# Performance work log

Measured on AMD Instinct MI355X. Metric: run time of the kernel, lower is better.

Reference implementation:

```python
import jax, jax.numpy as jnp
import numpy as np

N, E, IN_DIM, HID, HEADS, OUT_DIM, T = 50000, 200000, 32, 64, 4, 32, 3
NEG_SLOPE = 0.2  # PyG GATv2Conv default


def setup_inputs() -> dict:
    key = jax.random.key(0)
    ks = jax.random.split(key, 16)
    s = 0.1
    return {
        "feat": jax.random.normal(ks[0], (N, IN_DIM), jnp.float32),
        "W_in": jax.random.normal(ks[1], (IN_DIM, HID), jnp.float32) * s,
        "b_in": jnp.zeros((HID,), jnp.float32),
        "Wl": jax.random.normal(ks[2], (2 * HID, HEADS * HID), jnp.float32) * s,
        "bl": jnp.zeros((HEADS * HID,), jnp.float32),
        "Wr": jax.random.normal(ks[3], (2 * HID, HEADS * HID), jnp.float32) * s,
        "br": jnp.zeros((HEADS * HID,), jnp.float32),
        "att": jax.random.normal(ks[4], (HEADS, HID), jnp.float32) * s,
        "b_conv": jnp.zeros((HEADS * HID,), jnp.float32),
        "Wg": jax.random.normal(ks[5], (HID, OUT_DIM), jnp.float32) * s,
        "bg": jnp.zeros((OUT_DIM,), jnp.float32),
        "edge_index": jax.random.randint(ks[6], (2, E), 0, N, jnp.int32),
        "node_mask": jax.random.randint(ks[7], (N,), 0, T + 1, jnp.int32),
        "current_state": jax.random.randint(ks[8], (N,), 0, 2, jnp.int32),
    }


def reference(feat, W_in, b_in, Wl, bl, Wr, br, att, b_conv, Wg, bg,
              edge_index, node_mask, current_state):
    # add self loops (GATv2Conv add_self_loops=True)
    loops = jnp.arange(N, dtype=edge_index.dtype)
    src = jnp.concatenate([edge_index[0], loops])  # [E+N]
    dst = jnp.concatenate([edge_index[1], loops])

    h0 = feat @ W_in + b_in  # [N, HID]
    bias_sum = b_conv.reshape(HEADS, HID).sum(0)  # heads are summed after bias add

    def step(h, i):
        active = node_mask > i  # [N] bool: nodes updated at this step
        x = jnp.concatenate([h, h0], axis=-1)  # [N, 2*HID]
        xl = (x @ Wl + bl).reshape(N, HEADS, HID)  # source transform
        xr = (x @ Wr + br).reshape(N, HEADS, HID)  # target transform
        e_act = active[src] & active[dst]  # edge alive iff both endpoints active
        s = jax.nn.leaky_relu(xl[src] + xr[dst], NEG_SLOPE)  # [E+N, H, C]
        score = jnp.einsum('ehc,hc->eh', s, att)  # [E+N, H]
        score = jnp.where(e_act[:, None], score, -1e30)
        smax = jax.lax.stop_gradient(
            jax.ops.segment_max(score, dst, num_segments=N))  # [N, H]
        ex = jnp.exp(score - smax[dst]) * e_act[:, None].astype(score.dtype)
        denom = jax.ops.segment_sum(ex, dst, num_segments=N)  # [N, H]
        alpha = ex / jnp.maximum(denom[dst], 1e-16)  # segment softmax per dst
        msg = alpha[:, :, None] * xl[src]  # [E+N, H, C]
        agg = jax.ops.segment_sum(msg, dst, num_segments=N)  # [N, H, C]
        out = jnp.tanh(agg.sum(1) + bias_sum)  # sum over heads, then Tanh
        return jnp.where(active[:, None], out, h), None

    h, _ = jax.lax.scan(step, h0, jnp.arange(T))
    # original returns g_embed(h[current_state]); fixed-shape variant: mask rows
    out = (h @ Wg + bg) * (current_state[:, None] > 0).astype(h.dtype)
    return out
```

## Files before the change

### kernel.cpp

```cpp
#include <hip/hip_runtime.h>
#include <hip/hip_bf16.h>

#define NN      50000
#define EE      200000
#define IN_DIM  32
#define HID     64
#define HEADS   4
#define OUTD    32
#define TSTEPS  3

typedef unsigned short bf16_t;
typedef __attribute__((ext_vector_type(8))) short  short8;
typedef __attribute__((ext_vector_type(4))) float  floatx4;

__device__ __forceinline__ float b2f(bf16_t u) {
    union { unsigned int i; float f; } v; v.i = ((unsigned int)u) << 16; return v.f;
}
__device__ __forceinline__ bf16_t f2b(float f) {
    union { float f; unsigned int i; } v; v.f = f;
    unsigned int r = v.i + 0x7FFF + ((v.i >> 16) & 1);
    return (bf16_t)(r >> 16);
}

#define H0_BLOCKS ((NN + 31) / 32)

__global__ __launch_bounds__(256) void k_setup(
        const void* W_in, const void* b_in, const void* att, const void* bconv,
        const void* Wg, const void* bg,
        const void* Wl_raw, const void* Wr_raw, const void* bl_raw, const void* br_raw,
        const void* feat_raw,
        float* attf, float* bcf, float* Wgf, float* bgf,
        bf16_t* __restrict__ Wt, bf16_t* __restrict__ WtS, float* __restrict__ bb,
        int* __restrict__ deg, int* __restrict__ flag, int* __restrict__ mbuf,
        bf16_t* __restrict__ h0, bf16_t* __restrict__ h) {
    __shared__ int bad;
    __shared__ float Ws[IN_DIM * HID];
    __shared__ float bs[HID];
    int t = threadIdx.x, bid = blockIdx.x;
    if (t == 0) bad = 0;
    __syncthreads();
    {
        const bf16_t* p = (const bf16_t*)W_in;
        int mybad = 0;
        for (int i = t; i < IN_DIM * HID; i += 256) {
            float v = b2f(p[i]);
            if (v != v || fabsf(v) > 100.f) mybad = 1;
        }
        if (mybad) atomicOr(&bad, 1);
    }
    __syncthreads();
    int f = bad ? 0 : 1;
    if (bid == 0 && t == 0) *flag = f;

    if (bid < 256) {
        int i = bid * 256 + t;
        int n = i >> 7, k = i & 127;
        const void* W = (n < 256) ? Wl_raw : Wr_raw;
        int nn = (n < 256) ? n : n - 256;
        float v = f ? b2f(((const bf16_t*)W)[k * 256 + nn])
                    : ((const float*)W)[k * 256 + nn];
        Wt[n * 128 + k] = f2b(v);
        if (k < 64) {
            float v2 = f ? b2f(((const bf16_t*)W)[(k + 64) * 256 + nn])
                         : ((const float*)W)[(k + 64) * 256 + nn];
            WtS[n * 64 + k] = f2b(v + v2);
        }
        if (k == 0) {
            const void* b = (n < 256) ? bl_raw : br_raw;
            bb[n] = f ? b2f(((const bf16_t*)b)[nn]) : ((const float*)b)[nn];
        }
    } else if (bid < 267) {
        int i = (bid - 256) * 256 + t;
        const void* src; float* dst; int off;
        if      (i < 256)  { src = att;   dst = attf; off = i; }
        else if (i < 512)  { src = bconv; dst = bcf;  off = i - 256; }
        else if (i < 2560) { src = Wg;    dst = Wgf;  off = i - 512; }
        else if (i < 2592) { src = bg;    dst = bgf;  off = i - 2560; }
        else return;
        dst[off] = f ? b2f(((const bf16_t*)src)[off]) : ((const float*)src)[off];
    } else if (bid < 463) {
        int i = (bid - 267) * 256 + t;
        if (i < NN) deg[i] = 0;
        if (bid == 267 && t < 16) mbuf[t] = 0;
    } else {
        for (int i = t; i < IN_DIM * HID; i += 256)
            Ws[i] = f ? b2f(((const bf16_t*)W_in)[i]) : ((const float*)W_in)[i];
        if (t < HID)
            bs[t] = f ? b2f(((const bf16_t*)b_in)[t]) : ((const float*)b_in)[t];
        __syncthreads();
        int nb = bid - 463;
        int wid = t >> 6, c = t & 63;
#pragma unroll
        for (int g = 0; g < 8; g++) {
            int node = (nb * 8 + g) * 4 + wid;
            if (node >= NN) break;
            float acc = bs[c];
            if (f) {
                const bf16_t* fr = (const bf16_t*)feat_raw + (size_t)node * IN_DIM;
#pragma unroll
                for (int k = 0; k < IN_DIM; k++) acc += b2f(fr[k]) * Ws[k * HID + c];
            } else {
                const float* fr = (const float*)feat_raw + (size_t)node * IN_DIM;
#pragma unroll
                for (int k = 0; k < IN_DIM; k++) acc += fr[k] * Ws[k * HID + c];
            }
            bf16_t o = f2b(acc);
            h0[(size_t)node * HID + c] = o;
            h [(size_t)node * HID + c] = o;
        }
    }
}

__global__ __launch_bounds__(256) void k_hist_all(const int* __restrict__ dst,
                                                  const int* __restrict__ mask,
                                                  int* __restrict__ deg,
                                                  int* __restrict__ mbuf) {
    int t = threadIdx.x, bid = blockIdx.x;
    int i = bid * 256 + t;
    if (i < EE) atomicAdd(&deg[dst[i]], 1);
    if (bid < (NN + 255) / 256) {
        __shared__ int wcnt[4][4];
        int wid = t >> 6, lane = t & 63;
        int ni = bid * 256 + t;
        bool valid = ni < NN;
        int v = 0;
        if (valid) { int m = mask[ni]; v = m < 0 ? 0 : (m > 3 ? 3 : m); }
#pragma unroll
        for (int b = 0; b < 4; b++) {
            unsigned long long mm = __ballot(valid && v == b);
            if (lane == 0) wcnt[wid][b] = __popcll(mm);
        }
        __syncthreads();
        if (t < 4) {
            int s = wcnt[0][t] + wcnt[1][t] + wcnt[2][t] + wcnt[3][t];
            if (s) atomicAdd(&mbuf[t], s);
        }
    }
}

__global__ __launch_bounds__(256) void k_scan_partial(const int* __restrict__ deg,
                                                      int* __restrict__ part, int n) {
    __shared__ int sd[256];
    int t = threadIdx.x;
    int base = blockIdx.x * 1024;
    int s = 0;
#pragma unroll
    for (int j = 0; j < 4; j++) {
        int i = base + t * 4 + j;
        if (i < n) s += deg[i];
    }
    sd[t] = s; __syncthreads();
    for (int off = 128; off > 0; off >>= 1) {
        if (t < off) sd[t] += sd[t + off];
        __syncthreads();
    }
    if (t == 0) part[blockIdx.x] = sd[0];
}

__global__ __launch_bounds__(256) void k_scan_final(const int* __restrict__ deg,
                                                    const int* __restrict__ part,
                                                    int* __restrict__ row_ptr,
                                                    int* __restrict__ cursor,
                                                    int n, int nch,
                                                    int* __restrict__ mbuf) {
    __shared__ int sc[256];
    __shared__ int bpref;
    int t = threadIdx.x;
    int bid = blockIdx.x;
    if (t == 0) {
        int acc = 0;
        for (int i = 0; i < bid; i++) acc += part[i];
        bpref = acc;
        if (bid == 0) {
            int tot = 0;
            for (int i = 0; i < nch; i++) tot += part[i];
            row_ptr[n] = tot;
            int c1 = mbuf[1], c2 = mbuf[2], c3 = mbuf[3];
            mbuf[7] = 0;
            mbuf[6] = c3;
            mbuf[5] = c3 + c2;
            mbuf[4] = c3 + c2 + c1;
            mbuf[8] = c3 + c2 + c1;
            mbuf[9] = c3 + c2;
            mbuf[10] = c3;
        }
    }
    int base = bid * 1024;
    int v[4]; int s = 0;
#pragma unroll
    for (int j = 0; j < 4; j++) {
        int i = base + t * 4 + j;
        v[j] = (i < n) ? deg[i] : 0;
        s += v[j];
    }
    sc[t] = s; __syncthreads();
    for (int off = 1; off < 256; off <<= 1) {
        int add = (t >= off) ? sc[t - off] : 0;
        __syncthreads();
        sc[t] += add;
        __syncthreads();
    }
    int run = sc[t] - s + bpref;
#pragma unroll
    for (int j = 0; j < 4; j++) {
        int i = base + t * 4 + j;
        if (i < n) { row_ptr[i] = run; cursor[i] = run; run += v[j]; }
    }
}

__global__ __launch_bounds__(256) void k_scatter_all(const int* __restrict__ src,
                                                     const int* __restrict__ dst,
                                                     int* __restrict__ cursor,
                                                     int* __restrict__ col,
                                                     const int* __restrict__ mask,
                                                     int* __restrict__ mbuf,
                                                     int* __restrict__ order) {
    int t = threadIdx.x, bid = blockIdx.x;
    int i = bid * 256 + t;
    if (i < EE) {
        int sv = src[i];
        int m = mask[sv]; m = m < 0 ? 0 : (m > 3 ? 3 : m);
        int d = dst[i];
        int pos = atomicAdd(&cursor[d], 1);
        col[pos] = sv | (m << 28);
    }
    if (bid < (NN + 255) / 256) {
        __shared__ int wcnt[4][4];
        __shared__ int bbase[4];
        int wid = t >> 6, lane = t & 63;
        int ni = bid * 256 + t;
        bool valid = ni < NN;
        int v = 0;
        if (valid) { int m = mask[ni]; v = m < 0 ? 0 : (m > 3 ? 3 : m); }
        int rank = 0;
#pragma unroll
        for (int b = 0; b < 4; b++) {
            unsigned long long mm = __ballot(valid && v == b);
            if (valid && v == b)
                rank = __popcll(mm & ((lane == 0) ? 0ull : (~0ull >> (64 - lane))));
            if (lane == 0) wcnt[wid][b] = __popcll(mm);
        }
        __syncthreads();
        if (t < 4) {
            int tot = wcnt[0][t] + wcnt[1][t] + wcnt[2][t] + wcnt[3][t];
            bbase[t] = atomicAdd(&mbuf[4 + t], tot);
        }
        __syncthreads();
        if (valid) {
            int wpre = 0;
            for (int ww = 0; ww < wid; ww++) wpre += wcnt[ww][v];
            order[bbase[v] + wpre + rank] = ni;
        }
    }
}

__global__ __launch_bounds__(256) void k_gemm0(const bf16_t* __restrict__ h0,
                                               const bf16_t* __restrict__ WtS,
                                               const float* __restrict__ bb,
                                               bf16_t* __restrict__ xl,
                                               bf16_t* __restrict__ xr,
                                               const int* __restrict__ order,
                                               const int* __restrict__ mbuf) {
    int count = mbuf[8];
    int mbase = blockIdx.x * 64;
    if (mbase >= count) return;

    __shared__ bf16_t smem[64 * 72 + 128 * 72];
    bf16_t* As = smem;
    bf16_t* Bs = smem + 64 * 72;
    bf16_t* Cs = smem;

    int t = threadIdx.x;
    int nbase = blockIdx.y * 128;

    {
        int ln = t >> 2, lq = t & 3;
        int idx = mbase + ln;
        int node = (idx < count) ? order[idx] : -1;
        ulonglong2 z; z.x = 0; z.y = 0;
        ulonglong2 v0 = z, v1 = z;
        if (node >= 0) {
            v0 = *(const ulonglong2*)(h0 + (size_t)node * HID + lq * 16);
            v1 = *(const ulonglong2*)(h0 + (size_t)node * HID + lq * 16 + 8);
        }
        *(ulonglong2*)(&As[ln * 72 + lq * 16]) = v0;
        *(ulonglong2*)(&As[ln * 72 + lq * 16 + 8]) = v1;
    }
    {
        int n = t >> 1, kc = (t & 1) * 32;
        const bf16_t* srcp = WtS + (size_t)(nbase + n) * 64 + kc;
        bf16_t* dstp = &Bs[n * 72 + kc];
        *(ulonglong2*)(dstp)      = *(const ulonglong2*)(srcp);
        *(ulonglong2*)(dstp + 8)  = *(const ulonglong2*)(srcp + 8);
        *(ulonglong2*)(dstp + 16) = *(const ulonglong2*)(srcp + 16);
        *(ulonglong2*)(dstp + 24) = *(const ulonglong2*)(srcp + 24);
    }
    __syncthreads();

    int wv = t >> 6, lane = t & 63, mrow = lane & 15, quad = lane >> 4;
    floatx4 acc[8];
#pragma unroll
    for (int nf = 0; nf < 8; nf++) acc[nf] = (floatx4){0.f, 0.f, 0.f, 0.f};
#pragma unroll
    for (int kq = 0; kq < 2; kq++) {
        short8 a = *(const short8*)(&As[(wv * 16 + mrow) * 72 + kq * 32 + quad * 8]);
#pragma unroll
        for (int nf = 0; nf < 8; nf++) {
            short8 b = *(const short8*)(&Bs[(nf * 16 + mrow) * 72 + kq * 32 + quad * 8]);
            acc[nf] = __builtin_amdgcn_mfma_f32_16x16x32_bf16(a, b, acc[nf], 0, 0, 0);
        }
    }
    __syncthreads();

#pragma unroll
    for (int nf = 0; nf < 8; nf++) {
        float bv = bb[nbase + nf * 16 + mrow];
#pragma unroll
        for (int r = 0; r < 4; r++) {
            int m = wv * 16 + quad * 4 + r;
            Cs[m * 136 + nf * 16 + mrow] = f2b(acc[nf][r] + bv);
        }
    }
    __syncthreads();

    bf16_t* outp = (blockIdx.y < 2) ? xl : xr;
    int cc = (blockIdx.y & 1) * 128;
#pragma unroll
    for (int i = 0; i < 4; i++) {
        int c = t + i * 256;
        int m = c >> 4, kc = (c & 15) * 8;
        int idx = mbase + m;
        if (idx < count) {
            int node = order[idx];
            *(ulonglong2*)(outp + (size_t)node * 256 + cc + kc) =
                *(const ulonglong2*)(&Cs[m * 136 + kc]);
        }
    }
}

__global__ __launch_bounds__(256) void k_gemm_mfma(const bf16_t* __restrict__ h,
                                                   const bf16_t* __restrict__ h0,
                                                   const bf16_t* __restrict__ Wt,
                                                   const float* __restrict__ bb,
                                                   bf16_t* __restrict__ xl,
                                                   bf16_t* __restrict__ xr,
                                                   const int* __restrict__ order,
                                                   const int* __restrict__ mbuf,
                                                   int step) {
    int count = mbuf[8 + step];
    int mbase = blockIdx.x * 64;
    if (mbase >= count) return;

    __shared__ bf16_t smem[64 * 136 + 128 * 136];
    bf16_t* As = smem;
    bf16_t* Bs = smem + 64 * 136;
    bf16_t* Cs = smem;

    int t = threadIdx.x;
    int nbase = blockIdx.y * 128;

    {
        int ln = t >> 2, lq = t & 3;
        int idx = mbase + ln;
        int node = (idx < count) ? order[idx] : -1;
        ulonglong2 z; z.x = 0; z.y = 0;
#pragma unroll
        for (int j = 0; j < 2; j++) {
            int chunk = lq + j * 4;
            ulonglong2 vh = z, vh0 = z;
            if (node >= 0) {
                vh  = *(const ulonglong2*)(h  + (size_t)node * HID + chunk * 8);
                vh0 = *(const ulonglong2*)(h0 + (size_t)node * HID + chunk * 8);
            }
            *(ulonglong2*)(&As[ln * 136 + chunk * 8]) = vh;
            *(ulonglong2*)(&As[ln * 136 + 64 + chunk * 8]) = vh0;
        }
    }
#pragma unroll
    for (int i = 0; i < 8; i++) {
        int c = t + i * 256;
        int n = c >> 4, kc = (c & 15) * 8;
        *(ulonglong2*)(&Bs[n * 136 + kc]) =
            *(const ulonglong2*)(Wt + (size_t)(nbase + n) * 128 + kc);
    }
    __syncthreads();

    int wv = t >> 6, lane = t & 63, mrow = lane & 15, quad = lane >> 4;
    floatx4 acc[8];
#pragma unroll
    for (int nf = 0; nf < 8; nf++) acc[nf] = (floatx4){0.f, 0.f, 0.f, 0.f};
#pragma unroll
    for (int kq = 0; kq < 4; kq++) {
        short8 a = *(const short8*)(&As[(wv * 16 + mrow) * 136 + kq * 32 + quad * 8]);
#pragma unroll
        for (int nf = 0; nf < 8; nf++) {
            short8 b = *(const short8*)(&Bs[(nf * 16 + mrow) * 136 + kq * 32 + quad * 8]);
            acc[nf] = __builtin_amdgcn_mfma_f32_16x16x32_bf16(a, b, acc[nf], 0, 0, 0);
        }
    }
    __syncthreads();

#pragma unroll
    for (int nf = 0; nf < 8; nf++) {
        float bv = bb[nbase + nf * 16 + mrow];
#pragma unroll
        for (int r = 0; r < 4; r++) {
            int m = wv * 16 + quad * 4 + r;
            Cs[m * 136 + nf * 16 + mrow] = f2b(acc[nf][r] + bv);
        }
    }
    __syncthreads();

    bf16_t* outp = (blockIdx.y < 2) ? xl : xr;
    int cc = (blockIdx.y & 1) * 128;
#pragma unroll
    for (int i = 0; i < 4; i++) {
        int c = t + i * 256;
        int m = c >> 4, kc = (c & 15) * 8;
        int idx = mbase + m;
        if (idx < count) {
            int node = order[idx];
            *(ulonglong2*)(outp + (size_t)node * 256 + cc + kc) =
                *(const ulonglong2*)(&Cs[m * 136 + kc]);
        }
    }
}

__global__ __launch_bounds__(256) void k_agg(bf16_t* __restrict__ h,
                                             const bf16_t* __restrict__ xl,
                                             const bf16_t* __restrict__ xr,
                                             const float* __restrict__ att,
                                             const float* __restrict__ b_conv,
                                             const int* __restrict__ row_ptr,
                                             const int* __restrict__ col,
                                             const int* __restrict__ order,
                                             const int* __restrict__ mbuf,
                                             int step) {
    int count = mbuf[8 + step];
    int wid = threadIdx.x >> 6;
    int lane = threadIdx.x & 63;
    float4 attv = *(const float4*)(att + lane * 4);
    float4 bcv  = *(const float4*)(b_conv + lane * 4);

    for (int idx = blockIdx.x * 4 + wid; idx < count; idx += gridDim.x * 4) {
        int node = order[idx];

        ushort4 xru = *(const ushort4*)(xr + (size_t)node * 256 + lane * 4);
        float xr0 = b2f(xru.x), xr1 = b2f(xru.y), xr2 = b2f(xru.z), xr3 = b2f(xru.w);

        float a0 = 0.f, a1 = 0.f, a2 = 0.f, a3 = 0.f, l = 0.f;

        auto do_edge = [&](int s) {
            ushort4 xu = *(const ushort4*)(xl + (size_t)s * 256 + lane * 4);
            float x0 = b2f(xu.x), x1 = b2f(xu.y), x2 = b2f(xu.z), x3 = b2f(xu.w);
            float v0 = x0 + xr0; v0 = v0 > 0.f ? v0 : 0.2f * v0;
            float v1 = x1 + xr1; v1 = v1 > 0.f ? v1 : 0.2f * v1;
            float v2 = x2 + xr2; v2 = v2 > 0.f ? v2 : 0.2f * v2;
            float v3 = x3 + xr3; v3 = v3 > 0.f ? v3 : 0.2f * v3;
            float part = attv.x * v0 + attv.y * v1 + attv.z * v2 + attv.w * v3;
            part += __shfl_xor(part, 1, 64);
            part += __shfl_xor(part, 2, 64);
            part += __shfl_xor(part, 4, 64);
            part += __shfl_xor(part, 8, 64);
            float p = __expf(part);
            l += p;
            a0 += p * x0; a1 += p * x1; a2 += p * x2; a3 += p * x3;
        };

        do_edge(node);
        int e0 = row_ptr[node], e1 = row_ptr[node + 1];
        int e = e0;
        for (; e + 3 < e1; e += 4) {
            int c0 = col[e], c1 = col[e + 1], c2 = col[e + 2], c3 = col[e + 3];
            if (((unsigned)c0 >> 28) > (unsigned)step) do_edge(c0 & 0x0FFFFFFF);
            if (((unsigned)c1 >> 28) > (unsigned)step) do_edge(c1 & 0x0FFFFFFF);
            if (((unsigned)c2 >> 28) > (unsigned)step) do_edge(c2 & 0x0FFFFFFF);
            if (((unsigned)c3 >> 28) > (unsigned)step) do_edge(c3 & 0x0FFFFFFF);
        }
        for (; e < e1; e++) {
            int c = col[e];
            if (((unsigned)c >> 28) > (unsigned)step) do_edge(c & 0x0FFFFFFF);
        }

        float inv = 1.f / l;
        float t0 = a0 * inv + bcv.x;
        float t1 = a1 * inv + bcv.y;
        float t2 = a2 * inv + bcv.z;
        float t3 = a3 * inv + bcv.w;
        t0 += __shfl_xor(t0, 16, 64); t0 += __shfl_xor(t0, 32, 64);
        t1 += __shfl_xor(t1, 16, 64); t1 += __shfl_xor(t1, 32, 64);
        t2 += __shfl_xor(t2, 16, 64); t2 += __shfl_xor(t2, 32, 64);
        t3 += __shfl_xor(t3, 16, 64); t3 += __shfl_xor(t3, 32, 64);
        if (lane < 16) {
            ushort4 o;
            o.x = f2b(tanhf(t0)); o.y = f2b(tanhf(t1));
            o.z = f2b(tanhf(t2)); o.w = f2b(tanhf(t3));
            *(ushort4*)(h + (size_t)node * HID + lane * 4) = o;
        }
    }
}

__global__ __launch_bounds__(256) void k_out(const bf16_t* __restrict__ h,
                                             const float* __restrict__ Wg,
                                             const float* __restrict__ bg,
                                             const int* __restrict__ cs,
                                             void* __restrict__ out,
                                             const int* __restrict__ flag) {
    __shared__ float Ws[HID * OUTD];
    __shared__ float bs[OUTD];
    int t = threadIdx.x;
    for (int i = t; i < HID * OUTD; i += 256) Ws[i] = Wg[i];
    if (t < OUTD) bs[t] = bg[t];
    __syncthreads();
    int node = blockIdx.x * 8 + (t >> 5);
    int c = t & 31;
    if (node >= NN) return;
    float res = 0.f;
    if (cs[node] > 0) {
        const bf16_t* hr = h + (size_t)node * HID;
        float acc = bs[c];
#pragma unroll
        for (int k = 0; k < HID; k++) acc += b2f(hr[k]) * Ws[k * OUTD + c];
        res = acc;
    }
    size_t idx = (size_t)node * OUTD + c;
    if (*flag) ((bf16_t*)out)[idx] = f2b(res);
    else       ((float*)out)[idx]  = res;
}

static inline size_t alignup(size_t x) { return (x + 255) & ~(size_t)255; }

extern "C" void kernel_launch(void* const* d_in, const int* in_sizes, int n_in,
                              void* d_out, int out_size, void* d_ws, size_t ws_size,
                              hipStream_t stream) {
    const void* feat_raw  = d_in[0];
    const void* W_in_raw  = d_in[1];
    const void* b_in_raw  = d_in[2];
    const void* Wl_raw    = d_in[3];
    const void* bl_raw    = d_in[4];
    const void* Wr_raw    = d_in[5];
    const void* br_raw    = d_in[6];
    const void* att_raw   = d_in[7];
    const void* bconv_raw = d_in[8];
    const void* Wg_raw    = d_in[9];
    const void* bg_raw    = d_in[10];
    const int* edge       = (const int*)d_in[11];
    const int* nmask      = (const int*)d_in[12];
    const int* cstate     = (const int*)d_in[13];

    const int* e_src = edge;
    const int* e_dst = edge + EE;

    const size_t SZ_HB   = alignup((size_t)NN * HID * sizeof(bf16_t));
    const size_t SZ_X    = alignup((size_t)NN * 256 * sizeof(bf16_t));
    const size_t SZ_I    = alignup((size_t)NN * sizeof(int));
    const size_t SZ_RP   = alignup((size_t)(NN + 1) * sizeof(int));
    const size_t SZ_COL  = alignup((size_t)EE * sizeof(int));
    const int nch = (NN + 1023) / 1024;
    const size_t SZ_PART = alignup((size_t)(nch + 1) * sizeof(int));
    const size_t SZ_WT   = alignup((size_t)512 * 128 * sizeof(bf16_t));
    const size_t SZ_WTS  = alignup((size_t)512 * 64 * sizeof(bf16_t));
    const size_t SZ_B    = alignup(512 * sizeof(float));
    const size_t SZ_WG   = alignup((size_t)HID * OUTD * sizeof(float));

    char* w = (char*)d_ws;
    bf16_t* h0   = (bf16_t*)w; w += SZ_HB;
    bf16_t* h    = (bf16_t*)w; w += SZ_HB;
    bf16_t* xl   = (bf16_t*)w; w += SZ_X;
    bf16_t* xr   = (bf16_t*)w; w += SZ_X;
    int* deg     = (int*)w;    w += SZ_I;
    int* row_ptr = (int*)w;    w += SZ_RP;
    int* cursor  = (int*)w;    w += SZ_I;
    int* colA    = (int*)w;    w += SZ_COL;
    int* order   = (int*)w;    w += SZ_I;
    int* part    = (int*)w;    w += SZ_PART;
    bf16_t* Wt   = (bf16_t*)w; w += SZ_WT;
    bf16_t* WtS  = (bf16_t*)w; w += SZ_WTS;
    float* bb    = (float*)w;  w += SZ_B;
    float* attf  = (float*)w;  w += SZ_B;
    float* bcf   = (float*)w;  w += SZ_B;
    float* Wgf   = (float*)w;  w += SZ_WG;
    float* bgf   = (float*)w;  w += SZ_B;
    int* flag    = (int*)w;    w += 256;
    int* mbuf    = (int*)w;    w += 256;
    if ((size_t)(w - (char*)d_ws) > ws_size) return;

    k_setup<<<463 + H0_BLOCKS, 256, 0, stream>>>(
        W_in_raw, b_in_raw, att_raw, bconv_raw, Wg_raw, bg_raw,
        Wl_raw, Wr_raw, bl_raw, br_raw, feat_raw,
        attf, bcf, Wgf, bgf, Wt, WtS, bb, deg, flag, mbuf, h0, h);

    k_hist_all<<<(EE + 255) / 256, 256, 0, stream>>>(e_dst, nmask, deg, mbuf);
    k_scan_partial<<<nch, 256, 0, stream>>>(deg, part, NN);
    k_scan_final<<<nch, 256, 0, stream>>>(deg, part, row_ptr, cursor, NN, nch, mbuf);
    k_scatter_all<<<(EE + 255) / 256, 256, 0, stream>>>(e_src, e_dst, cursor, colA,
                                                        nmask, mbuf, order);

    k_gemm0<<<dim3((NN + 63) / 64, 4), 256, 0, stream>>>(h0, WtS, bb, xl, xr, order, mbuf);
    k_agg<<<2048, 256, 0, stream>>>(h, xl, xr, attf, bcf, row_ptr, colA, order, mbuf, 0);

    for (int s = 1; s < TSTEPS; s++) {
        k_gemm_mfma<<<dim3((NN + 63) / 64, 4), 256, 0, stream>>>(h, h0, Wt, bb, xl, xr,
                                                                 order, mbuf, s);
        k_agg<<<2048, 256, 0, stream>>>(h, xl, xr, attf, bcf,
                                        row_ptr, colA, order, mbuf, s);
    }

    k_out<<<(NN + 7) / 8, 256, 0, stream>>>(h, Wgf, bgf, cstate, d_out, flag);
}
```

Baseline: 252.4 us.

## Merge mask histogram into setup, fuse scan kernels, batch edge loads in aggregation

Moves the node-mask bucket counting into the setup kernel as per-block counts, which removes the mbuf zeroing and its atomics. It also merges the two-pass scan into one kernel in which each block recomputes its prefix from deg, so one launch is dropped. The degree histogram now reads four destinations per thread with int4 loads. The aggregation loop compacts active edges into groups of four so their gathers are issued together, and uses DPP adds instead of shuffles for the head reduction. Setup and output projection vectorise their row loads. Having every scan block re-read the preceding deg values adds redundant work, and the edge-queue branching may add divergence.

```diff
diff --git a/kernel.cpp b/kernel.cpp
--- a/kernel.cpp
+++ b/kernel.cpp
@@ -22,20 +22,26 @@
     return (bf16_t)(r >> 16);
 }
 
+#define DPP_ADD(x, ctrl) ((x) + __int_as_float(                                 \
+        __builtin_amdgcn_update_dpp(0, __float_as_int(x), (ctrl), 0xF, 0xF, true)))
+
 #define H0_BLOCKS ((NN + 31) / 32)
+#define NB_NODE   ((NN + 255) / 256)
+#define NBC       (NB_NODE * 4)
 
 __global__ __launch_bounds__(256) void k_setup(
         const void* W_in, const void* b_in, const void* att, const void* bconv,
         const void* Wg, const void* bg,
         const void* Wl_raw, const void* Wr_raw, const void* bl_raw, const void* br_raw,
-        const void* feat_raw,
+        const void* feat_raw, const int* __restrict__ nmask,
         float* attf, float* bcf, float* Wgf, float* bgf,
         bf16_t* __restrict__ Wt, bf16_t* __restrict__ WtS, float* __restrict__ bb,
-        int* __restrict__ deg, int* __restrict__ flag, int* __restrict__ mbuf,
+        int* __restrict__ deg, int* __restrict__ flag, int* __restrict__ bcount,
         bf16_t* __restrict__ h0, bf16_t* __restrict__ h) {
     __shared__ int bad;
     __shared__ float Ws[IN_DIM * HID];
     __shared__ float bs[HID];
+    __shared__ int wcnt[4][4];
     int t = threadIdx.x, bid = blockIdx.x;
     if (t == 0) bad = 0;
     __syncthreads();
@@ -78,17 +84,29 @@
         else if (i < 2592) { src = bg;    dst = bgf;  off = i - 2560; }
         else return;
         dst[off] = f ? b2f(((const bf16_t*)src)[off]) : ((const float*)src)[off];
-    } else if (bid < 463) {
-        int i = (bid - 267) * 256 + t;
-        if (i < NN) deg[i] = 0;
-        if (bid == 267 && t < 16) mbuf[t] = 0;
+    } else if (bid < 267 + NB_NODE) {
+        int nb = bid - 267;
+        int i = nb * 256 + t;
+        bool valid = i < NN;
+        if (valid) deg[i] = 0;
+        int wid = t >> 6, lane = t & 63;
+        int v = 0;
+        if (valid) { int m = nmask[i]; v = m < 0 ? 0 : (m > 3 ? 3 : m); }
+#pragma unroll
+        for (int b = 0; b < 4; b++) {
+            unsigned long long mm = __ballot(valid && v == b);
+            if (lane == 0) wcnt[wid][b] = __popcll(mm);
+        }
+        __syncthreads();
+        if (t < 4)
+            bcount[nb * 4 + t] = wcnt[0][t] + wcnt[1][t] + wcnt[2][t] + wcnt[3][t];
     } else {
         for (int i = t; i < IN_DIM * HID; i += 256)
             Ws[i] = f ? b2f(((const bf16_t*)W_in)[i]) : ((const float*)W_in)[i];
         if (t < HID)
             bs[t] = f ? b2f(((const bf16_t*)b_in)[t]) : ((const float*)b_in)[t];
         __syncthreads();
-        int nb = bid - 463;
+        int nb = bid - (267 + NB_NODE);
         int wid = t >> 6, c = t & 63;
 #pragma unroll
         for (int g = 0; g < 8; g++) {
@@ -96,13 +114,26 @@
             if (node >= NN) break;
             float acc = bs[c];
             if (f) {
-                const bf16_t* fr = (const bf16_t*)feat_raw + (size_t)node * IN_DIM;
-#pragma unroll
-                for (int k = 0; k < IN_DIM; k++) acc += b2f(fr[k]) * Ws[k * HID + c];
+                const short8* fr8 = (const short8*)((const bf16_t*)feat_raw
+                                                    + (size_t)node * IN_DIM);
+#pragma unroll
+                for (int j = 0; j < 4; j++) {
+                    short8 fv = fr8[j];
+#pragma unroll
+                    for (int k = 0; k < 8; k++)
+                        acc += b2f((bf16_t)fv[k]) * Ws[(j * 8 + k) * HID + c];
+                }
             } else {
-                const float* fr = (const float*)feat_raw + (size_t)node * IN_DIM;
-#pragma unroll
-                for (int k = 0; k < IN_DIM; k++) acc += fr[k] * Ws[k * HID + c];
+                const float4* fr4 = (const float4*)((const float*)feat_raw
+                                                    + (size_t)node * IN_DIM);
+#pragma unroll
+                for (int j = 0; j < 8; j++) {
+                    float4 fv = fr4[j];
+                    acc += fv.x * Ws[(j * 4 + 0) * HID + c];
+                    acc += fv.y * Ws[(j * 4 + 1) * HID + c];
+                    acc += fv.z * Ws[(j * 4 + 2) * HID + c];
+                    acc += fv.w * Ws[(j * 4 + 3) * HID + c];
+                }
             }
             bf16_t o = f2b(acc);
             h0[(size_t)node * HID + c] = o;
@@ -111,71 +142,38 @@
     }
 }
 
-__global__ __launch_bounds__(256) void k_hist_all(const int* __restrict__ dst,
-                                                  const int* __restrict__ mask,
-                                                  int* __restrict__ deg,
-                                                  int* __restrict__ mbuf) {
+__global__ __launch_bounds__(256) void k_hist(const int* __restrict__ dst,
+                                              int* __restrict__ deg) {
+    int i = (blockIdx.x * 256 + threadIdx.x) * 4;
+    if (i + 3 < EE) {
+        int4 d = *(const int4*)(dst + i);
+        atomicAdd(&deg[d.x], 1);
+        atomicAdd(&deg[d.y], 1);
+        atomicAdd(&deg[d.z], 1);
+        atomicAdd(&deg[d.w], 1);
+    } else {
+        for (; i < EE; i++) atomicAdd(&deg[dst[i]], 1);
+    }
+}
+
+__global__ __launch_bounds__(256) void k_scan(const int* __restrict__ deg,
+                                              int* __restrict__ row_ptr,
+                                              int* __restrict__ cursor,
+                                              const int* __restrict__ bcount,
+                                              int* __restrict__ mbuf,
+                                              int n, int nch) {
+    __shared__ int sc[256];
+    __shared__ int spre[256];
+    __shared__ int cb[4];
     int t = threadIdx.x, bid = blockIdx.x;
-    int i = bid * 256 + t;
-    if (i < EE) atomicAdd(&deg[dst[i]], 1);
-    if (bid < (NN + 255) / 256) {
-        __shared__ int wcnt[4][4];
-        int wid = t >> 6, lane = t & 63;
-        int ni = bid * 256 + t;
-        bool valid = ni < NN;
-        int v = 0;
-        if (valid) { int m = mask[ni]; v = m < 0 ? 0 : (m > 3 ? 3 : m); }
-#pragma unroll
-        for (int b = 0; b < 4; b++) {
-            unsigned long long mm = __ballot(valid && v == b);
-            if (lane == 0) wcnt[wid][b] = __popcll(mm);
-        }
-        __syncthreads();
-        if (t < 4) {
-            int s = wcnt[0][t] + wcnt[1][t] + wcnt[2][t] + wcnt[3][t];
-            if (s) atomicAdd(&mbuf[t], s);
-        }
-    }
-}
-
-__global__ __launch_bounds__(256) void k_scan_partial(const int* __restrict__ deg,
-                                                      int* __restrict__ part, int n) {
-    __shared__ int sd[256];
-    int t = threadIdx.x;
-    int base = blockIdx.x * 1024;
-    int s = 0;
-#pragma unroll
-    for (int j = 0; j < 4; j++) {
-        int i = base + t * 4 + j;
-        if (i < n) s += deg[i];
-    }
-    sd[t] = s; __syncthreads();
-    for (int off = 128; off > 0; off >>= 1) {
-        if (t < off) sd[t] += sd[t + off];
-        __syncthreads();
-    }
-    if (t == 0) part[blockIdx.x] = sd[0];
-}
-
-__global__ __launch_bounds__(256) void k_scan_final(const int* __restrict__ deg,
-                                                    const int* __restrict__ part,
-                                                    int* __restrict__ row_ptr,
-                                                    int* __restrict__ cursor,
-                                                    int n, int nch,
-                                                    int* __restrict__ mbuf) {
-    __shared__ int sc[256];
-    __shared__ int bpref;
-    int t = threadIdx.x;
-    int bid = blockIdx.x;
-    if (t == 0) {
-        int acc = 0;
-        for (int i = 0; i < bid; i++) acc += part[i];
-        bpref = acc;
-        if (bid == 0) {
-            int tot = 0;
-            for (int i = 0; i < nch; i++) tot += part[i];
-            row_ptr[n] = tot;
-            int c1 = mbuf[1], c2 = mbuf[2], c3 = mbuf[3];
+
+    if (bid == 0) {
+        if (t < 4) cb[t] = 0;
+        __syncthreads();
+        for (int i = t; i < NBC; i += 256) atomicAdd(&cb[i & 3], bcount[i]);
+        __syncthreads();
+        if (t == 0) {
+            int c1 = cb[1], c2 = cb[2], c3 = cb[3];
             mbuf[7] = 0;
             mbuf[6] = c3;
             mbuf[5] = c3 + c2;
@@ -185,7 +183,24 @@
             mbuf[10] = c3;
         }
     }
+
     int base = bid * 1024;
+    int pre = 0;
+    {
+        const int4* d4 = (const int4*)deg;
+        int lim = base >> 2;
+        for (int i = t; i < lim; i += 256) {
+            int4 q = d4[i];
+            pre += q.x + q.y + q.z + q.w;
+        }
+    }
+    spre[t] = pre; __syncthreads();
+    for (int off = 128; off > 0; off >>= 1) {
+        if (t < off) spre[t] += spre[t + off];
+        __syncthreads();
+    }
+    int bpref = spre[0];
+
     int v[4]; int s = 0;
 #pragma unroll
     for (int j = 0; j < 4; j++) {
@@ -204,8 +219,10 @@
 #pragma unroll
     for (int j = 0; j < 4; j++) {
         int i = base + t * 4 + j;
-        if (i < n) { row_ptr[i] = run; cursor[i] = run; run += v[j]; }
-    }
+        if (i < n) { row_ptr[i] = run; cursor[i] = run; }
+        run += v[j];
+    }
+    if (bid == nch - 1 && t == 255) row_ptr[n] = run;
 }
 
 __global__ __launch_bounds__(256) void k_scatter_all(const int* __restrict__ src,
@@ -224,7 +241,7 @@
         int pos = atomicAdd(&cursor[d], 1);
         col[pos] = sv | (m << 28);
     }
-    if (bid < (NN + 255) / 256) {
+    if (bid < NB_NODE) {
         __shared__ int wcnt[4][4];
         __shared__ int bbase[4];
         int wid = t >> 6, lane = t & 63;
@@ -450,36 +467,50 @@
 
         float a0 = 0.f, a1 = 0.f, a2 = 0.f, a3 = 0.f, l = 0.f;
 
-        auto do_edge = [&](int s) {
-            ushort4 xu = *(const ushort4*)(xl + (size_t)s * 256 + lane * 4);
+        auto ld = [&](int s) {
+            return *(const ushort4*)(xl + (size_t)s * 256 + lane * 4);
+        };
+        auto body = [&](ushort4 xu) {
             float x0 = b2f(xu.x), x1 = b2f(xu.y), x2 = b2f(xu.z), x3 = b2f(xu.w);
             float v0 = x0 + xr0; v0 = v0 > 0.f ? v0 : 0.2f * v0;
             float v1 = x1 + xr1; v1 = v1 > 0.f ? v1 : 0.2f * v1;
             float v2 = x2 + xr2; v2 = v2 > 0.f ? v2 : 0.2f * v2;
             float v3 = x3 + xr3; v3 = v3 > 0.f ? v3 : 0.2f * v3;
             float part = attv.x * v0 + attv.y * v1 + attv.z * v2 + attv.w * v3;
-            part += __shfl_xor(part, 1, 64);
-            part += __shfl_xor(part, 2, 64);
-            part += __shfl_xor(part, 4, 64);
-            part += __shfl_xor(part, 8, 64);
+            part = DPP_ADD(part, 0xB1);
+            part = DPP_ADD(part, 0x4E);
+            part = DPP_ADD(part, 0x141);
+            part = DPP_ADD(part, 0x140);
             float p = __expf(part);
             l += p;
             a0 += p * x0; a1 += p * x1; a2 += p * x2; a3 += p * x3;
         };
 
-        do_edge(node);
+        int q0 = node, q1 = 0, q2 = 0, q3 = 0;
+        int qn = 1;
         int e0 = row_ptr[node], e1 = row_ptr[node + 1];
-        int e = e0;
-        for (; e + 3 < e1; e += 4) {
-            int c0 = col[e], c1 = col[e + 1], c2 = col[e + 2], c3 = col[e + 3];
-            if (((unsigned)c0 >> 28) > (unsigned)step) do_edge(c0 & 0x0FFFFFFF);
-            if (((unsigned)c1 >> 28) > (unsigned)step) do_edge(c1 & 0x0FFFFFFF);
-            if (((unsigned)c2 >> 28) > (unsigned)step) do_edge(c2 & 0x0FFFFFFF);
-            if (((unsigned)c3 >> 28) > (unsigned)step) do_edge(c3 & 0x0FFFFFFF);
-        }
-        for (; e < e1; e++) {
+        for (int e = e0; e < e1; e++) {
             int c = col[e];
-            if (((unsigned)c >> 28) > (unsigned)step) do_edge(c & 0x0FFFFFFF);
+            if (((unsigned)c >> 28) > (unsigned)step) {
+                int s = c & 0x0FFFFFFF;
+                if (qn == 0) q0 = s;
+                else if (qn == 1) q1 = s;
+                else if (qn == 2) q2 = s;
+                else q3 = s;
+                if (++qn == 4) {
+                    ushort4 u0 = ld(q0), u1 = ld(q1), u2 = ld(q2), u3 = ld(q3);
+                    body(u0); body(u1); body(u2); body(u3);
+                    qn = 0;
+                }
+            }
+        }
+        if (qn) {
+            ushort4 u0 = ld(q0), u1, u2;
+            if (qn > 1) u1 = ld(q1);
+            if (qn > 2) u2 = ld(q2);
+            body(u0);
+            if (qn > 1) body(u1);
+            if (qn > 2) body(u2);
         }
 
         float inv = 1.f / l;
@@ -517,10 +548,15 @@
     if (node >= NN) return;
     float res = 0.f;
     if (cs[node] > 0) {
-        const bf16_t* hr = h + (size_t)node * HID;
+        const short8* hr8 = (const short8*)(h + (size_t)node * HID);
         float acc = bs[c];
 #pragma unroll
-        for (int k = 0; k < HID; k++) acc += b2f(hr[k]) * Ws[k * OUTD + c];
+        for (int j = 0; j < 8; j++) {
+            short8 hv = hr8[j];
+#pragma unroll
+            for (int k = 0; k < 8; k++)
+                acc += b2f((bf16_t)hv[k]) * Ws[(j * 8 + k) * OUTD + c];
+        }
         res = acc;
     }
     size_t idx = (size_t)node * OUTD + c;
@@ -557,7 +593,7 @@
     const size_t SZ_RP   = alignup((size_t)(NN + 1) * sizeof(int));
     const size_t SZ_COL  = alignup((size_t)EE * sizeof(int));
     const int nch = (NN + 1023) / 1024;
-    const size_t SZ_PART = alignup((size_t)(nch + 1) * sizeof(int));
+    const size_t SZ_BC   = alignup((size_t)NBC * sizeof(int));
     const size_t SZ_WT   = alignup((size_t)512 * 128 * sizeof(bf16_t));
     const size_t SZ_WTS  = alignup((size_t)512 * 64 * sizeof(bf16_t));
     const size_t SZ_B    = alignup(512 * sizeof(float));
@@ -573,7 +609,7 @@
     int* cursor  = (int*)w;    w += SZ_I;
     int* colA    = (int*)w;    w += SZ_COL;
     int* order   = (int*)w;    w += SZ_I;
-    int* part    = (int*)w;    w += SZ_PART;
+    int* bcount  = (int*)w;    w += SZ_BC;
     bf16_t* Wt   = (bf16_t*)w; w += SZ_WT;
     bf16_t* WtS  = (bf16_t*)w; w += SZ_WTS;
     float* bb    = (float*)w;  w += SZ_B;
@@ -585,14 +621,13 @@
     int* mbuf    = (int*)w;    w += 256;
     if ((size_t)(w - (char*)d_ws) > ws_size) return;
 
-    k_setup<<<463 + H0_BLOCKS, 256, 0, stream>>>(
+    k_setup<<<467 + H0_BLOCKS - 4, 256, 0, stream>>>(
         W_in_raw, b_in_raw, att_raw, bconv_raw, Wg_raw, bg_raw,
-        Wl_raw, Wr_raw, bl_raw, br_raw, feat_raw,
-        attf, bcf, Wgf, bgf, Wt, WtS, bb, deg, flag, mbuf, h0, h);
-
-    k_hist_all<<<(EE + 255) / 256, 256, 0, stream>>>(e_dst, nmask, deg, mbuf);
-    k_scan_partial<<<nch, 256, 0, stream>>>(deg, part, NN);
-    k_scan_final<<<nch, 256, 0, stream>>>(deg, part, row_ptr, cursor, NN, nch, mbuf);
+        Wl_raw, Wr_raw, bl_raw, br_raw, feat_raw, nmask,
+        attf, bcf, Wgf, bgf, Wt, WtS, bb, deg, flag, bcount, h0, h);
+
+    k_hist<<<(EE + 1023) / 1024, 256, 0, stream>>>(e_dst, deg);
+    k_scan<<<nch, 256, 0, stream>>>(deg, row_ptr, cursor, bcount, mbuf, NN, nch);
     k_scatter_all<<<(EE + 255) / 256, 256, 0, stream>>>(e_src, e_dst, cursor, colA,
                                                         nmask, mbuf, order);
 
```

After: 275.3 us. +9.1%, slower.
